# Kernel optimization log

Measured on AMD Instinct MI355X. Metric: run time of the kernel, lower is better.

Reference implementation:

```python
import jax, jax.numpy as jnp
import numpy as np

S = 16   # num_states
C = 8    # input_channels
B = 64   # batch
L = 4096 # sequence length


def hyperbolic_sigmoid(x):
    return x / (1 + jnp.abs(x)) * 0.5 + 0.5


def hyperbolic_softmax(logits, axis):
    x = hyperbolic_sigmoid(logits)
    return x / jnp.sum(x, axis=axis, keepdims=True)


def setup_inputs() -> dict:
    key = jax.random.key(0)
    k0, k1, k2, k3 = jax.random.split(key, 4)
    return {
        "log_input_probs": jax.random.normal(k0, (B, L, C), dtype=jnp.float32),
        "invh_initial_state_probs": jax.random.normal(k1, (S,), dtype=jnp.float32),
        "invh_transition_probs": jax.random.normal(k2, (S, C, S), dtype=jnp.float32),
        "invh_accepting_state_probs": jax.random.normal(k3, (S,), dtype=jnp.float32),
    }


def reference(log_input_probs, invh_initial_state_probs, invh_transition_probs, invh_accepting_state_probs):
    # hyperbolic parameterization -> probabilities
    initial_state_probs = hyperbolic_softmax(invh_initial_state_probs, axis=0)         # (S,)
    transition_probs = hyperbolic_softmax(invh_transition_probs, axis=2)               # (S,C,S)
    accepting_state_logprobs = jnp.log(hyperbolic_sigmoid(invh_accepting_state_probs)) # (S,)

    input_probs = jnp.exp(log_input_probs)  # (B,L,C)
    # per-timestep transition matrices, (B,L,S,S)
    trans_each = jnp.einsum('pcn,blc->blpn', transition_probs, input_probs)
    # log-depth chain product m0 @ m1 @ ... @ m_{L-1} via associative scan
    prefix = jax.lax.associative_scan(jnp.matmul, trans_each, axis=1)
    transition_overall = prefix[:, -1]  # (B,S,S)
    # p_state[b,n] = sum_p overall[b,p,n] * init[p]
    p_state = jnp.einsum('bpn,p->bn', transition_overall, initial_state_probs)
    log_p_state = jnp.log(p_state + 1e-20)
    log_acceptance = jax.nn.logsumexp(log_p_state + accepting_state_logprobs[None, :], axis=1)  # (B,)
    return log_acceptance[None]  # (1,B)
```

## Files before the change

kernel.cpp:

```cpp
#include <hip/hip_runtime.h>
#include <math.h>

#define S 16
#define C 8
#define NB 64
#define L 4096
#define K 64
#define LC 64

#define SLOT 324
#define RS 20

typedef __attribute__((ext_vector_type(8))) short bf16x8;
typedef __attribute__((ext_vector_type(4))) short bf16x4;
typedef __attribute__((ext_vector_type(4))) float f32x4;
typedef unsigned long long ull;

#define WS_INIT 0
#define WS_ACC  64
#define WS_CLOG 512
#define WS_TTT  16896
#define WS_CP   49664

__device__ __forceinline__ float hsig(float x) {
    return x / (1.0f + fabsf(x)) * 0.5f + 0.5f;
}
__device__ __forceinline__ unsigned short f2bf(float f) {
    unsigned int u = __float_as_uint(f);
    return (unsigned short)((u + 0x7fffu + ((u >> 16) & 1u)) >> 16);
}

__device__ __forceinline__ bf16x8 ldfrag(const unsigned short* base, int lane) {
    int col = lane & 15, quad = lane >> 4;
    bf16x8 f = {0, 0, 0, 0, 0, 0, 0, 0};
    if (quad < 2) {
        const bf16x4* p = (const bf16x4*)(base + col * RS + quad * 8);
        bf16x4 lo = p[0], hi = p[1];
        f[0] = lo[0]; f[1] = lo[1]; f[2] = lo[2]; f[3] = lo[3];
        f[4] = hi[0]; f[5] = hi[1]; f[6] = hi[2]; f[7] = hi[3];
    }
    return f;
}

__device__ __forceinline__ f32x4 prod2(const unsigned short* slots, int sa, int sb, int lane) {
    bf16x8 a = ldfrag(slots + sa * SLOT, lane);
    bf16x8 b = ldfrag(slots + sb * SLOT, lane);
    f32x4 c = {0.f, 0.f, 0.f, 0.f};
    return __builtin_amdgcn_mfma_f32_16x16x32_bf16(a, b, c, 0, 0, 0);
}

__device__ __forceinline__ bf16x8 ldfrag_g(const unsigned short* base, int lane) {
    int col = lane & 15, quad = lane >> 4;
    bf16x8 f = {0, 0, 0, 0, 0, 0, 0, 0};
    if (quad < 2) f = *(const bf16x8*)(base + col * 16 + quad * 8);
    return f;
}

__device__ __forceinline__ void store16(unsigned short* slot, f32x4 d, int lane, bool odd) {
    int col = lane & 15, quad = lane >> 4;
    if (odd) {
        ull pk = (ull)f2bf(d[0]) | ((ull)f2bf(d[1]) << 16)
               | ((ull)f2bf(d[2]) << 32) | ((ull)f2bf(d[3]) << 48);
        *(ull*)(slot + col * RS + quad * 4) = pk;
    } else {
#pragma unroll
        for (int r = 0; r < 4; r++) slot[(quad * 4 + r) * RS + col] = f2bf(d[r]);
    }
}

__device__ __forceinline__ f32x4 tree32_inplace(unsigned short* slots, int lane, int w) {
#pragma unroll
    for (int i2 = 0; i2 < 4; i2++) {
        int i = 4 * w + i2;
        store16(slots + (2 * i) * SLOT, prod2(slots, 2 * i, 2 * i + 1, lane), lane, i & 1);
    }
#pragma unroll
    for (int i2 = 0; i2 < 2; i2++) {
        int i = 2 * w + i2;
        store16(slots + (4 * i) * SLOT, prod2(slots, 4 * i, 4 * i + 2, lane), lane, i & 1);
    }
    store16(slots + (8 * w) * SLOT, prod2(slots, 8 * w, 8 * w + 4, lane), lane, w & 1);
    __syncthreads();
    if (w < 2)
        store16(slots + (16 * w) * SLOT, prod2(slots, 16 * w, 16 * w + 8, lane), lane, w & 1);
    __syncthreads();
    return prod2(slots, 0, 16, lane);
}

__global__ void __launch_bounds__(256) prepall_kernel(const float* __restrict__ invh_init,
                                                      const float* __restrict__ invh_T,
                                                      const float* __restrict__ invh_acc,
                                                      unsigned char* __restrict__ wsb) {
    __shared__ float Tn[2048];
    int t = threadIdx.x;
    int cc = blockIdx.x, c = cc >> 3, c2 = cc & 7;
    if (t < S * C) {
        float v[S]; float s = 0.f;
#pragma unroll
        for (int n = 0; n < S; n++) { v[n] = hsig(invh_T[t * S + n]); s += v[n]; }
        float inv = 1.f / s;
#pragma unroll
        for (int n = 0; n < S; n++) Tn[t * S + n] = v[n] * inv;
    }
    __syncthreads();
    int p = t >> 4, n = t & 15;
    float a = 0.f;
#pragma unroll
    for (int k = 0; k < S; k++) a += Tn[(p * 8 + c) * 16 + k] * Tn[(k * 8 + c2) * 16 + n];
    ((unsigned short*)(wsb + WS_TTT))[t * 64 + cc] = f2bf(a);

    if (cc == 0 && t < S) {
        float s = 0.f;
#pragma unroll
        for (int k = 0; k < S; k++) s += hsig(invh_init[k]);
        ((float*)(wsb + WS_INIT))[t] = hsig(invh_init[t]) / s;
        ((float*)(wsb + WS_ACC))[t] = logf(hsig(invh_acc[t]));
    }
}

__global__ void __launch_bounds__(256) chunk_kernel(const float* __restrict__ logx,
                                                    unsigned char* __restrict__ wsb) {
    __shared__ __align__(16) unsigned short slots[32 * SLOT];
    __shared__ float xs[2 * LC * C];

    int tid = threadIdx.x, lane = tid & 63, w = tid >> 6;
    int col = lane & 15, quad = lane >> 4;
    int chunk = blockIdx.x, b = blockIdx.y;

    const unsigned short* TTT = (const unsigned short*)(wsb + WS_TTT);
    bf16x8 bfr[4][2];
#pragma unroll
    for (int jj = 0; jj < 4; jj++) {
        int t = 4 * w + jj;
#pragma unroll
        for (int kk = 0; kk < 2; kk++)
            bfr[jj][kk] = *(const bf16x8*)(TTT + (t * 16 + col) * 64 + kk * 32 + quad * 8);
    }

    const float* xg = logx + ((size_t)b * L + (size_t)chunk * LC) * C;
    xs[tid] = xg[tid];
    xs[tid + 256] = xg[tid + 256];
    __syncthreads();

    if (tid < LC) {
        float v[C]; float m = -INFINITY;
#pragma unroll
        for (int c = 0; c < C; c++) { v[c] = xs[tid * C + c]; m = fmaxf(m, v[c]); }
        float s = 0.f;
#pragma unroll
        for (int c = 0; c < C; c++) { v[c] = __expf(v[c] - m); s += v[c]; }
        float lx = m + __logf(s);
        float inv = 1.0f / s;
#pragma unroll
        for (int c = 0; c < C; c++) xs[tid * C + c] = v[c] * inv;
        float cl = lx;
#pragma unroll
        for (int d = 1; d < 64; d <<= 1) cl += __shfl_xor(cl, d);
        if (lane == 0) ((float*)(wsb + WS_CLOG))[b * K + chunk] = cl;
    }
    __syncthreads();

    bf16x8 afr[2][2];
#pragma unroll
    for (int mt = 0; mt < 2; mt++) {
        int i2 = 2 * (mt * 16 + col);
        const float4* x1p = (const float4*)(xs + (i2 + 1) * 8);
        float4 xa = x1p[0], xb = x1p[1];
#pragma unroll
        for (int kk = 0; kk < 2; kk++) {
            float x0 = xs[i2 * 8 + kk * 4 + quad];
            bf16x8 a;
            a[0] = (short)f2bf(x0 * xa.x); a[1] = (short)f2bf(x0 * xa.y);
            a[2] = (short)f2bf(x0 * xa.z); a[3] = (short)f2bf(x0 * xa.w);
            a[4] = (short)f2bf(x0 * xb.x); a[5] = (short)f2bf(x0 * xb.y);
            a[6] = (short)f2bf(x0 * xb.z); a[7] = (short)f2bf(x0 * xb.w);
            afr[mt][kk] = a;
        }
    }

#pragma unroll
    for (int mt = 0; mt < 2; mt++)
#pragma unroll
        for (int jj = 0; jj < 4; jj++) {
            f32x4 acc = {0.f, 0.f, 0.f, 0.f};
#pragma unroll
            for (int kk = 0; kk < 2; kk++)
                acc = __builtin_amdgcn_mfma_f32_16x16x32_bf16(afr[mt][kk], bfr[jj][kk], acc, 0, 0, 0);
            int t = 4 * w + jj;
#pragma unroll
            for (int r = 0; r < 4; r++) {
                int i = mt * 16 + quad * 4 + r;
                int off = (i & 1) ? (col * RS + t) : (t * RS + col);
                slots[i * SLOT + off] = f2bf(acc[r]);
            }
        }
    __syncthreads();

    f32x4 root = tree32_inplace(slots, lane, w);

    if (w == 0) {
        unsigned short* cp = (unsigned short*)(wsb + WS_CP) + ((size_t)b * K + chunk) * 256;
        if (chunk & 1) {
            ull pk = (ull)f2bf(root[0]) | ((ull)f2bf(root[1]) << 16)
                   | ((ull)f2bf(root[2]) << 32) | ((ull)f2bf(root[3]) << 48);
            *(ull*)(cp + col * 16 + quad * 4) = pk;
        } else {
#pragma unroll
            for (int r = 0; r < 4; r++) cp[(quad * 4 + r) * 16 + col] = f2bf(root[r]);
        }
    }
}

__global__ void __launch_bounds__(256) reduce_kernel(unsigned char* __restrict__ wsb,
                                                     float* __restrict__ out) {
    __shared__ __align__(16) unsigned short slots[32 * SLOT];
    int tid = threadIdx.x, lane = tid & 63, w = tid >> 6;
    int col = lane & 15, quad = lane >> 4;
    int b = blockIdx.x;

    const unsigned short* cpb = (const unsigned short*)(wsb + WS_CP) + (size_t)b * K * 256;
#pragma unroll
    for (int i2 = 0; i2 < 8; i2++) {
        int i = 8 * w + i2;
        bf16x8 a  = ldfrag_g(cpb + (size_t)(2 * i) * 256, lane);
        bf16x8 bb = ldfrag_g(cpb + (size_t)(2 * i + 1) * 256, lane);
        f32x4 c0 = {0.f, 0.f, 0.f, 0.f};
        f32x4 d = __builtin_amdgcn_mfma_f32_16x16x32_bf16(a, bb, c0, 0, 0, 0);
        store16(slots + i * SLOT, d, lane, i & 1);
    }

    f32x4 troot = tree32_inplace(slots, lane, w);

    if (w == 0) {
        const float* initp = (const float*)(wsb + WS_INIT);
        const float* acclog = (const float*)(wsb + WS_ACC);
        float part = 0.f;
#pragma unroll
        for (int r = 0; r < 4; r++) part += initp[quad * 4 + r] * troot[r];
        part += __shfl_xor(part, 16);
        part += __shfl_xor(part, 32);
        float lp = logf(fmaxf(part, 0.f) + 1e-30f) + acclog[col];
        float mx = lp;
#pragma unroll
        for (int d = 1; d < 16; d <<= 1) mx = fmaxf(mx, __shfl_xor(mx, d));
        float a2 = isfinite(mx) ? mx : 0.0f;
        float sm = expf(lp - a2);
#pragma unroll
        for (int d = 1; d < 16; d <<= 1) sm += __shfl_xor(sm, d);
        float cl = ((const float*)(wsb + WS_CLOG))[b * K + lane];
#pragma unroll
        for (int d = 1; d < 64; d <<= 1) cl += __shfl_xor(cl, d);
        if (lane == 0) out[b] = logf(sm) + a2 + cl;
    }
}

extern "C" void kernel_launch(void* const* d_in, const int* in_sizes, int n_in,
                              void* d_out, int out_size, void* d_ws, size_t ws_size,
                              hipStream_t stream) {
    const float* logx = (const float*)d_in[0];
    const float* init = (const float*)d_in[1];
    const float* T    = (const float*)d_in[2];
    const float* acc  = (const float*)d_in[3];
    unsigned char* wsb = (unsigned char*)d_ws;
    float* out = (float*)d_out;

    prepall_kernel<<<64, 256, 0, stream>>>(init, T, acc, wsb);
    chunk_kernel<<<dim3(K, NB), 256, 0, stream>>>(logx, wsb);
    reduce_kernel<<<NB, 256, 0, stream>>>(wsb, out);
}
```

Measured before the change: 92.39 us.

## Fuse chunk and reduce kernels via last-block atomic counter, use 16x16x16 MFMA

Merges the per-batch reduction into the chunk kernel: each block bumps a per-batch atomic counter, and the last block to finish does the final tree product, which removes one kernel launch. The 16x16x32 MFMA with half-zero operands is replaced by the 16x16x16 bf16 instruction. Some tree levels keep the product in registers as the B operand instead of writing it to LDS. The log-normalisation is parallelised across all threads with shuffles. Risks include the cost of the fences and atomics, and correctness depends on the counter being reset by the prep kernel.

```diff
diff --git a/kernel.cpp b/kernel.cpp
--- a/kernel.cpp
+++ b/kernel.cpp
@@ -18,6 +18,7 @@
 
 #define WS_INIT 0
 #define WS_ACC  64
+#define WS_CNT  128
 #define WS_CLOG 512
 #define WS_TTT  16896
 #define WS_CP   49664
@@ -30,32 +31,28 @@
     return (unsigned short)((u + 0x7fffu + ((u >> 16) & 1u)) >> 16);
 }
 
-__device__ __forceinline__ bf16x8 ldfrag(const unsigned short* base, int lane) {
-    int col = lane & 15, quad = lane >> 4;
-    bf16x8 f = {0, 0, 0, 0, 0, 0, 0, 0};
-    if (quad < 2) {
-        const bf16x4* p = (const bf16x4*)(base + col * RS + quad * 8);
-        bf16x4 lo = p[0], hi = p[1];
-        f[0] = lo[0]; f[1] = lo[1]; f[2] = lo[2]; f[3] = lo[3];
-        f[4] = hi[0]; f[5] = hi[1]; f[6] = hi[2]; f[7] = hi[3];
-    }
-    return f;
-}
-
-__device__ __forceinline__ f32x4 prod2(const unsigned short* slots, int sa, int sb, int lane) {
-    bf16x8 a = ldfrag(slots + sa * SLOT, lane);
-    bf16x8 b = ldfrag(slots + sb * SLOT, lane);
-    f32x4 c = {0.f, 0.f, 0.f, 0.f};
-    return __builtin_amdgcn_mfma_f32_16x16x32_bf16(a, b, c, 0, 0, 0);
-}
-
-__device__ __forceinline__ bf16x8 ldfrag_g(const unsigned short* base, int lane) {
-    int col = lane & 15, quad = lane >> 4;
-    bf16x8 f = {0, 0, 0, 0, 0, 0, 0, 0};
-    if (quad < 2) f = *(const bf16x8*)(base + col * 16 + quad * 8);
-    return f;
-}
-
+__device__ __forceinline__ f32x4 mfma16(bf16x4 a, bf16x4 b, f32x4 c) {
+#if __has_builtin(__builtin_amdgcn_mfma_f32_16x16x16bf16_1k)
+    return __builtin_amdgcn_mfma_f32_16x16x16bf16_1k(a, b, c, 0, 0, 0);
+#else
+    bf16x8 a8 = {a[0], a[1], a[2], a[3], 0, 0, 0, 0};
+    bf16x8 b8 = {b[0], b[1], b[2], b[3], 0, 0, 0, 0};
+    return __builtin_amdgcn_mfma_f32_16x16x32_bf16(a8, b8, c, 0, 0, 0);
+#endif
+}
+
+__device__ __forceinline__ bf16x4 ldfrag4(const unsigned short* base, int lane) {
+    return *(const bf16x4*)(base + (lane & 15) * RS + (lane >> 4) * 4);
+}
+__device__ __forceinline__ bf16x4 ldfrag_g4(const unsigned short* base, int lane) {
+    return *(const bf16x4*)(base + (lane & 15) * 16 + (lane >> 4) * 4);
+}
+__device__ __forceinline__ bf16x4 cvt4(f32x4 d) {
+    bf16x4 r;
+    r[0] = (short)f2bf(d[0]); r[1] = (short)f2bf(d[1]);
+    r[2] = (short)f2bf(d[2]); r[3] = (short)f2bf(d[3]);
+    return r;
+}
 __device__ __forceinline__ void store16(unsigned short* slot, f32x4 d, int lane, bool odd) {
     int col = lane & 15, quad = lane >> 4;
     if (odd) {
@@ -68,23 +65,23 @@
     }
 }
 
-__device__ __forceinline__ f32x4 tree32_inplace(unsigned short* slots, int lane, int w) {
-#pragma unroll
-    for (int i2 = 0; i2 < 4; i2++) {
-        int i = 4 * w + i2;
-        store16(slots + (2 * i) * SLOT, prod2(slots, 2 * i, 2 * i + 1, lane), lane, i & 1);
-    }
-#pragma unroll
-    for (int i2 = 0; i2 < 2; i2++) {
-        int i = 2 * w + i2;
-        store16(slots + (4 * i) * SLOT, prod2(slots, 4 * i, 4 * i + 2, lane), lane, i & 1);
-    }
-    store16(slots + (8 * w) * SLOT, prod2(slots, 8 * w, 8 * w + 4, lane), lane, w & 1);
-    __syncthreads();
-    if (w < 2)
-        store16(slots + (16 * w) * SLOT, prod2(slots, 16 * w, 16 * w + 8, lane), lane, w & 1);
-    __syncthreads();
-    return prod2(slots, 0, 16, lane);
+__device__ __forceinline__ f32x4 tree_upper(unsigned short* slots, int lane, int w,
+                                            bf16x4 B1a, bf16x4 B1b) {
+    f32x4 z = {0.f, 0.f, 0.f, 0.f};
+    f32x4 dA = mfma16(ldfrag4(slots + (8 * w) * SLOT, lane), B1a, z);
+    store16(slots + (8 * w) * SLOT, dA, lane, false);
+    f32x4 dB = mfma16(ldfrag4(slots + (8 * w + 4) * SLOT, lane), B1b, z);
+    bf16x4 B2 = cvt4(dB);
+    f32x4 d3 = mfma16(ldfrag4(slots + (8 * w) * SLOT, lane), B2, z);
+    store16(slots + (8 * w) * SLOT, d3, lane, w & 1);
+    __syncthreads();
+    if (w < 2) {
+        f32x4 d4 = mfma16(ldfrag4(slots + (16 * w) * SLOT, lane),
+                          ldfrag4(slots + (16 * w + 8) * SLOT, lane), z);
+        store16(slots + (16 * w) * SLOT, d4, lane, w & 1);
+    }
+    __syncthreads();
+    return mfma16(ldfrag4(slots, lane), ldfrag4(slots + 16 * SLOT, lane), z);
 }
 
 __global__ void __launch_bounds__(256) prepall_kernel(const float* __restrict__ invh_init,
@@ -109,19 +106,25 @@
     for (int k = 0; k < S; k++) a += Tn[(p * 8 + c) * 16 + k] * Tn[(k * 8 + c2) * 16 + n];
     ((unsigned short*)(wsb + WS_TTT))[t * 64 + cc] = f2bf(a);
 
-    if (cc == 0 && t < S) {
-        float s = 0.f;
-#pragma unroll
-        for (int k = 0; k < S; k++) s += hsig(invh_init[k]);
-        ((float*)(wsb + WS_INIT))[t] = hsig(invh_init[t]) / s;
-        ((float*)(wsb + WS_ACC))[t] = logf(hsig(invh_acc[t]));
-    }
-}
-
-__global__ void __launch_bounds__(256) chunk_kernel(const float* __restrict__ logx,
-                                                    unsigned char* __restrict__ wsb) {
+    if (cc == 0) {
+        if (t < K) ((int*)(wsb + WS_CNT))[t] = 0;
+        if (t < S) {
+            float s = 0.f;
+#pragma unroll
+            for (int k = 0; k < S; k++) s += hsig(invh_init[k]);
+            ((float*)(wsb + WS_INIT))[t] = hsig(invh_init[t]) / s;
+            ((float*)(wsb + WS_ACC))[t] = logf(hsig(invh_acc[t]));
+        }
+    }
+}
+
+__global__ void __launch_bounds__(256) main_kernel(const float* __restrict__ logx,
+                                                   unsigned char* __restrict__ wsb,
+                                                   float* __restrict__ out) {
     __shared__ __align__(16) unsigned short slots[32 * SLOT];
-    __shared__ float xs[2 * LC * C];
+    __shared__ __align__(16) float xs[LC * C];
+    __shared__ float clpart[4];
+    __shared__ int lastFlag;
 
     int tid = threadIdx.x, lane = tid & 63, w = tid >> 6;
     int col = lane & 15, quad = lane >> 4;
@@ -138,27 +141,23 @@
     }
 
     const float* xg = logx + ((size_t)b * L + (size_t)chunk * LC) * C;
-    xs[tid] = xg[tid];
-    xs[tid + 256] = xg[tid + 256];
-    __syncthreads();
-
-    if (tid < LC) {
-        float v[C]; float m = -INFINITY;
-#pragma unroll
-        for (int c = 0; c < C; c++) { v[c] = xs[tid * C + c]; m = fmaxf(m, v[c]); }
-        float s = 0.f;
-#pragma unroll
-        for (int c = 0; c < C; c++) { v[c] = __expf(v[c] - m); s += v[c]; }
-        float lx = m + __logf(s);
-        float inv = 1.0f / s;
-#pragma unroll
-        for (int c = 0; c < C; c++) xs[tid * C + c] = v[c] * inv;
-        float cl = lx;
-#pragma unroll
-        for (int d = 1; d < 64; d <<= 1) cl += __shfl_xor(cl, d);
-        if (lane == 0) ((float*)(wsb + WS_CLOG))[b * K + chunk] = cl;
-    }
-    __syncthreads();
+    float2 v = *(const float2*)(xg + 2 * tid);
+    float m = fmaxf(v.x, v.y);
+    m = fmaxf(m, __shfl_xor(m, 1));
+    m = fmaxf(m, __shfl_xor(m, 2));
+    float e0 = __expf(v.x - m), e1 = __expf(v.y - m);
+    float s = e0 + e1;
+    s += __shfl_xor(s, 1);
+    s += __shfl_xor(s, 2);
+    float inv = 1.0f / s;
+    *(float2*)(xs + 2 * tid) = make_float2(e0 * inv, e1 * inv);
+    float lx = ((tid & 3) == 0) ? (m + __logf(s)) : 0.f;
+#pragma unroll
+    for (int d = 1; d < 64; d <<= 1) lx += __shfl_xor(lx, d);
+    if (lane == 0) clpart[w] = lx;
+    __syncthreads();
+    if (tid == 0)
+        ((float*)(wsb + WS_CLOG))[b * K + chunk] = clpart[0] + clpart[1] + clpart[2] + clpart[3];
 
     bf16x8 afr[2][2];
 #pragma unroll
@@ -196,7 +195,19 @@
         }
     __syncthreads();
 
-    f32x4 root = tree32_inplace(slots, lane, w);
+    bf16x4 B1[2];
+    {
+        f32x4 z = {0.f, 0.f, 0.f, 0.f};
+#pragma unroll
+        for (int i2 = 0; i2 < 4; i2++) {
+            int i = 4 * w + i2;
+            f32x4 d = mfma16(ldfrag4(slots + (2 * i) * SLOT, lane),
+                             ldfrag4(slots + (2 * i + 1) * SLOT, lane), z);
+            if (i2 & 1) B1[i2 >> 1] = cvt4(d);
+            else store16(slots + (2 * i) * SLOT, d, lane, false);
+        }
+    }
+    f32x4 root = tree_upper(slots, lane, w, B1[0], B1[1]);
 
     if (w == 0) {
         unsigned short* cp = (unsigned short*)(wsb + WS_CP) + ((size_t)b * K + chunk) * 256;
@@ -208,28 +219,39 @@
 #pragma unroll
             for (int r = 0; r < 4; r++) cp[(quad * 4 + r) * 16 + col] = f2bf(root[r]);
         }
-    }
-}
-
-__global__ void __launch_bounds__(256) reduce_kernel(unsigned char* __restrict__ wsb,
-                                                     float* __restrict__ out) {
-    __shared__ __align__(16) unsigned short slots[32 * SLOT];
-    int tid = threadIdx.x, lane = tid & 63, w = tid >> 6;
-    int col = lane & 15, quad = lane >> 4;
-    int b = blockIdx.x;
-
+        __threadfence();
+    }
+    __syncthreads();
+    if (tid == 0) lastFlag = (atomicAdd((int*)(wsb + WS_CNT) + b, 1) == 63) ? 1 : 0;
+    __syncthreads();
+    if (!lastFlag) return;
+
+    __threadfence();
     const unsigned short* cpb = (const unsigned short*)(wsb + WS_CP) + (size_t)b * K * 256;
-#pragma unroll
-    for (int i2 = 0; i2 < 8; i2++) {
-        int i = 8 * w + i2;
-        bf16x8 a  = ldfrag_g(cpb + (size_t)(2 * i) * 256, lane);
-        bf16x8 bb = ldfrag_g(cpb + (size_t)(2 * i + 1) * 256, lane);
-        f32x4 c0 = {0.f, 0.f, 0.f, 0.f};
-        f32x4 d = __builtin_amdgcn_mfma_f32_16x16x32_bf16(a, bb, c0, 0, 0, 0);
-        store16(slots + i * SLOT, d, lane, i & 1);
-    }
-
-    f32x4 troot = tree32_inplace(slots, lane, w);
+    bf16x4 B0[4];
+    {
+        f32x4 z = {0.f, 0.f, 0.f, 0.f};
+#pragma unroll
+        for (int i2 = 0; i2 < 8; i2++) {
+            int j = 8 * w + i2;
+            f32x4 d = mfma16(ldfrag_g4(cpb + (size_t)(2 * j) * 256, lane),
+                             ldfrag_g4(cpb + (size_t)(2 * j + 1) * 256, lane), z);
+            if (i2 & 1) B0[i2 >> 1] = cvt4(d);
+            else store16(slots + j * SLOT, d, lane, false);
+        }
+    }
+    bf16x4 B1r[2];
+    {
+        f32x4 z = {0.f, 0.f, 0.f, 0.f};
+#pragma unroll
+        for (int i2 = 0; i2 < 4; i2++) {
+            int i = 4 * w + i2;
+            f32x4 d = mfma16(ldfrag4(slots + (2 * i) * SLOT, lane), B0[i2], z);
+            if (i2 & 1) B1r[i2 >> 1] = cvt4(d);
+            else store16(slots + (2 * i) * SLOT, d, lane, false);
+        }
+    }
+    f32x4 troot = tree_upper(slots, lane, w, B1r[0], B1r[1]);
 
     if (w == 0) {
         const float* initp = (const float*)(wsb + WS_INIT);
@@ -265,6 +287,5 @@
     float* out = (float*)d_out;
 
     prepall_kernel<<<64, 256, 0, stream>>>(init, T, acc, wsb);
-    chunk_kernel<<<dim3(K, NB), 256, 0, stream>>>(logx, wsb);
-    reduce_kernel<<<NB, 256, 0, stream>>>(wsb, out);
-}
+    main_kernel<<<dim3(K, NB), 256, 0, stream>>>(logx, wsb, out);
+}
```

After: 210.8 us. 128% more time.
